# Performance work log

Hardware: AMD Instinct MI355X
Metric: run time of the kernel (lower is better)

Reference implementation:

```python
import jax, jax.numpy as jnp
import numpy as np

NPG = 100          # nodes per graph
NUM_GRAPHS = 500
N = NPG * NUM_GRAPHS
DEG = 32
E = N * DEG
IN_DIM = 100
HID = 64           # out_channels / hidden_dim
HEADS = 2
NCLS = 2


def setup_inputs() -> dict:
    key = jax.random.key(0)
    ks = jax.random.split(key, 24)
    rng = np.random.default_rng(0)
    # edges within each graph, guaranteed no self-loops
    dst = np.repeat(np.arange(N), DEG)
    off = rng.integers(1, NPG, size=E)
    src = (dst // NPG) * NPG + ((dst % NPG) + off) % NPG
    edge_index = jnp.asarray(np.stack([src, dst]).astype(np.int32))
    batch = jnp.asarray((np.arange(N) // NPG).astype(np.int32))
    HC = HEADS * HID
    p = lambda k, sh: jax.random.normal(k, sh, jnp.float32) * 0.1
    return dict(
        x=jax.random.normal(ks[0], (N, IN_DIM), jnp.float32),
        edge_attr=jax.random.uniform(ks[1], (E,), jnp.float32),
        W1=p(ks[2], (IN_DIM, HC)), as1=p(ks[3], (HEADS, HID)), ad1=p(ks[4], (HEADS, HID)), bg1=p(ks[5], (HC,)),
        l1W=p(ks[6], (HC, HID)), l1b=p(ks[7], (HID,)), g1=jnp.ones((HID,), jnp.float32), b1=jnp.zeros((HID,), jnp.float32),
        W2=p(ks[8], (HID, HC)), as2=p(ks[9], (HEADS, HID)), ad2=p(ks[10], (HEADS, HID)), bg2=p(ks[11], (HC,)),
        l2W=p(ks[12], (HC, HID)), l2b=p(ks[13], (HID,)), g2=jnp.ones((HID,), jnp.float32), b2=jnp.zeros((HID,), jnp.float32),
        f1W=p(ks[14], (HID, HID)), f1b=p(ks[15], (HID,)),
        f2W=p(ks[16], (HID, HID // 2)), f2b=p(ks[17], (HID // 2,)),
        f3W=p(ks[18], (HID // 2, NCLS)), f3b=p(ks[19], (NCLS,)),
        edge_index=edge_index, batch=batch)


def reference(x, edge_attr, W1, as1, ad1, bg1, l1W, l1b, g1, b1,
              W2, as2, ad2, bg2, l2W, l2b, g2, b2,
              f1W, f1b, f2W, f2b, f3W, f3b, edge_index, batch):
    n = x.shape[0]
    ea = jnp.abs(edge_attr)  # computed as in forward; unused by attention_weighted variant
    # GATConv adds self-loops (fill doesn't matter for alpha-only message)
    sl = jnp.arange(n, dtype=edge_index.dtype)
    src = jnp.concatenate([edge_index[0], sl])
    dst = jnp.concatenate([edge_index[1], sl])
    lrelu = lambda z: jax.nn.leaky_relu(z, 0.2)

    def gat(h, W, a_s, a_d, bias):
        xp = (h @ W).reshape(n, HEADS, HID)                 # [N,H,C]
        e = lrelu(jnp.sum(xp * a_s, -1)[src] + jnp.sum(xp * a_d, -1)[dst])  # [E',H]
        m = jax.ops.segment_max(e, dst, num_segments=n)
        ex = jnp.exp(e - m[dst])
        alpha = ex / jax.ops.segment_sum(ex, dst, num_segments=n)[dst]      # edge softmax per dst
        out = jax.ops.segment_sum(xp[src] * alpha[:, :, None], dst, num_segments=n)
        return out.reshape(n, HEADS * HID) + bias

    def bn(z, g, b):  # BatchNorm1d with batch statistics (biased var, eps=1e-5)
        return (z - z.mean(0)) * jax.lax.rsqrt(z.var(0) + 1e-5) * g + b

    z = bn(lrelu(gat(x, W1, as1, ad1, bg1) @ l1W + l1b), g1, b1)
    z = bn(lrelu(gat(z, W2, as2, ad2, bg2) @ l2W + l2b), g2, b2)
    # global mean pool
    s = jax.ops.segment_sum(z, batch, num_segments=NUM_GRAPHS)
    cnt = jax.ops.segment_sum(jnp.ones((n, 1), z.dtype), batch, num_segments=NUM_GRAPHS)
    z = s / cnt
    z = lrelu(z @ f1W + f1b)
    z = lrelu(z @ f2W + f2b)
    return z @ f3W + f3b
```

## Files before the change

kernel.cpp:

```cpp
#include <hip/hip_runtime.h>

#define NN 50000
#define NPGc 100
#define NG 500
#define DEG 32
#define HC 128
#define HID 64

__device__ __forceinline__ float lrelu(float x) { return x > 0.0f ? x : 0.2f * x; }

__global__ void k_prep(const float* __restrict__ W1, const float* __restrict__ as1,
                       const float* __restrict__ ad1, float* __restrict__ Wa1,
                       const float* __restrict__ W2, const float* __restrict__ as2,
                       const float* __restrict__ ad2, float* __restrict__ Wa2) {
  const float* W  = blockIdx.x ? W2 : W1;
  const float* as_ = blockIdx.x ? as2 : as1;
  const float* ad_ = blockIdx.x ? ad2 : ad1;
  float* Wa = blockIdx.x ? Wa2 : Wa1;
  int K = blockIdx.x ? 64 : 100;
  int t = threadIdx.x;
  for (int u = t; u < K * 4; u += blockDim.x) {
    int k = u >> 2, s = u & 3;
    const float* a = (s < 2) ? as_ : ad_;
    int h = s & 1;
    float acc = 0.f;
    for (int c = 0; c < 64; ++c) acc += W[k * 128 + h * 64 + c] * a[h * 64 + c];
    Wa[k * 4 + s] = acc;
  }
}

template <int K, bool BN>
__global__ __launch_bounds__(256) void k_layer(
    const float* __restrict__ in, const float* __restrict__ W,
    const float* __restrict__ Wa, const float* __restrict__ AB,
    const int* __restrict__ esrc, const float* __restrict__ bg,
    float* __restrict__ gout) {
  constexpr int KP = (K % 32 == 0) ? K + 4 : K;
  __shared__ __align__(16) float xph[NPGc * 64];
  __shared__ __align__(16) char ubuf[NPGc * KP * 4];
  float* xin = (float*)ubuf;
  unsigned short* srcl = (unsigned short*)ubuf;
  float* sc = (float*)(ubuf + 6400);
  float* alpha = (float*)(ubuf + 7232);

  int t = threadIdx.x;
  int g = blockIdx.x >> 1, h = blockIdx.x & 1;
  int base = g * NPGc;

  constexpr int RQ = K / 4;
  for (int u = t; u < NPGc * RQ; u += 256) {
    int r = u / RQ, q = u % RQ;
    float4 v = ((const float4*)(in + (size_t)(base + r) * K))[q];
    if (BN) {
      float4 a4 = ((const float4*)AB)[q];
      float4 b4 = ((const float4*)(AB + 64))[q];
      v.x = v.x * a4.x + b4.x; v.y = v.y * a4.y + b4.y;
      v.z = v.z * a4.z + b4.z; v.w = v.w * a4.w + b4.w;
    }
    ((float4*)(xin + r * KP))[q] = v;
  }
  __syncthreads();

  int ng = t >> 4, cg = t & 15;
  {
    float4 acc[7];
#pragma unroll
    for (int i = 0; i < 7; ++i) acc[i] = make_float4(0.f, 0.f, 0.f, 0.f);
    const float4* W4 = (const float4*)W;
    float4 w4 = W4[h * 16 + cg];
    for (int k = 0; k < K; ++k) {
      float4 wc = w4;
      if (k + 1 < K) w4 = W4[(k + 1) * 32 + h * 16 + cg];
#pragma unroll
      for (int i = 0; i < 7; ++i) {
        int r = ng + 16 * i;
        if (r < NPGc) {
          float a = xin[r * KP + k];
          acc[i].x += a * wc.x; acc[i].y += a * wc.y;
          acc[i].z += a * wc.z; acc[i].w += a * wc.w;
        }
      }
    }
#pragma unroll
    for (int i = 0; i < 7; ++i) {
      int r = ng + 16 * i;
      if (r < NPGc) ((float4*)xph)[r * 16 + cg] = acc[i];
    }
  }
  float myscore = 0.f;
  if (t < 200) {
    int node = t >> 1, s = t & 1;
    for (int k = 0; k < K; ++k) myscore += xin[node * KP + k] * Wa[k * 4 + s * 2 + h];
  }
  __syncthreads();

  if (t < 200) sc[(t & 1) * NPGc + (t >> 1)] = myscore;
  for (int u = t; u < NPGc * DEG; u += 256)
    srcl[u] = (unsigned short)(esrc[base * DEG + u] - base);
  __syncthreads();

  if (t < NPGc) {
    float sd = sc[NPGc + t];
    float es = lrelu(sc[t] + sd);
    float m = es;
    float e[DEG];
#pragma unroll
    for (int j = 0; j < DEG; ++j) {
      e[j] = lrelu(sc[srcl[t * DEG + j]] + sd);
      m = fmaxf(m, e[j]);
    }
    float exs = __expf(es - m);
    float den = exs;
#pragma unroll
    for (int j = 0; j < DEG; ++j) { e[j] = __expf(e[j] - m); den += e[j]; }
    float inv = 1.0f / den;
    float* al = alpha + t * (DEG + 2);
#pragma unroll
    for (int j = 0; j < DEG; ++j) al[j] = e[j] * inv;
    al[DEG] = exs * inv;
  }
  __syncthreads();

  float4 bgv = ((const float4*)bg)[h * 16 + cg];
  for (int d = ng; d < NPGc; d += 16) {
    const float* al = alpha + d * (DEG + 2);
    const unsigned short* sp = srcl + d * DEG;
    float aself = al[DEG];
    float4 x4 = ((float4*)xph)[d * 16 + cg];
    float4 acc;
    acc.x = aself * x4.x; acc.y = aself * x4.y;
    acc.z = aself * x4.z; acc.w = aself * x4.w;
#pragma unroll 8
    for (int j = 0; j < DEG; ++j) {
      float a = al[j];
      float4 v = ((float4*)xph)[(int)sp[j] * 16 + cg];
      acc.x += a * v.x; acc.y += a * v.y;
      acc.z += a * v.z; acc.w += a * v.w;
    }
    acc.x += bgv.x; acc.y += bgv.y; acc.z += bgv.z; acc.w += bgv.w;
    ((float4*)gout)[(size_t)(base + d) * 32 + h * 16 + cg] = acc;
  }
}

__global__ __launch_bounds__(256) void k_out_gemm(
    const float* __restrict__ gin, const float* __restrict__ lW,
    const float* __restrict__ lb, float* __restrict__ h,
    float* __restrict__ partial) {
  __shared__ __align__(16) float gl[64 * 132];
  __shared__ float psum[2 * HID];
  int t = threadIdx.x;
  int n0 = blockIdx.x * 64;

  for (int u = t; u < 64 * 32; u += 256) {
    int r = u >> 5, q = u & 31;
    int n = n0 + r;
    float4 v = make_float4(0.f, 0.f, 0.f, 0.f);
    if (n < NN) v = ((const float4*)(gin + (size_t)n * HC))[q];
    ((float4*)(gl + r * 132))[q] = v;
  }
  if (t < 2 * HID) psum[t] = 0.f;
  __syncthreads();

  int ng = t >> 4, cg = t & 15;
  int r0 = ng * 4;
  float4 acc[4];
#pragma unroll
  for (int i = 0; i < 4; ++i) acc[i] = make_float4(0.f, 0.f, 0.f, 0.f);

  const float4* lW4 = (const float4*)lW;
  float4 w4 = lW4[cg];
  for (int k = 0; k < HC; ++k) {
    float4 wc = w4;
    if (k + 1 < HC) w4 = lW4[(k + 1) * 16 + cg];
#pragma unroll
    for (int i = 0; i < 4; ++i) {
      float a = gl[(r0 + i) * 132 + k];
      acc[i].x += a * wc.x; acc[i].y += a * wc.y;
      acc[i].z += a * wc.z; acc[i].w += a * wc.w;
    }
  }
  float4 bias = ((const float4*)lb)[cg];
  float s0 = 0, s1 = 0, s2 = 0, s3 = 0, q0 = 0, q1 = 0, q2 = 0, q3 = 0;
#pragma unroll
  for (int i = 0; i < 4; ++i) {
    int n = n0 + r0 + i;
    if (n < NN) {
      float4 v;
      v.x = lrelu(acc[i].x + bias.x); v.y = lrelu(acc[i].y + bias.y);
      v.z = lrelu(acc[i].z + bias.z); v.w = lrelu(acc[i].w + bias.w);
      ((float4*)(h + (size_t)n * HID))[cg] = v;
      s0 += v.x; q0 += v.x * v.x; s1 += v.y; q1 += v.y * v.y;
      s2 += v.z; q2 += v.z * v.z; s3 += v.w; q3 += v.w * v.w;
    }
  }
  int c0 = cg * 4;
  atomicAdd(&psum[c0 + 0], s0); atomicAdd(&psum[c0 + 1], s1);
  atomicAdd(&psum[c0 + 2], s2); atomicAdd(&psum[c0 + 3], s3);
  atomicAdd(&psum[HID + c0 + 0], q0); atomicAdd(&psum[HID + c0 + 1], q1);
  atomicAdd(&psum[HID + c0 + 2], q2); atomicAdd(&psum[HID + c0 + 3], q3);
  __syncthreads();
  if (t < 2 * HID) partial[blockIdx.x * 128 + t] = psum[t];
}

__global__ __launch_bounds__(256) void k_stats(
    const float* __restrict__ partial, int nb, const float* __restrict__ gamma,
    const float* __restrict__ beta, float* __restrict__ AB) {
  __shared__ float red[2][256];
  int c = blockIdx.x, t = threadIdx.x;
  float s = 0.f, sq = 0.f;
  for (int i = t; i < nb; i += 256) {
    s += partial[i * 128 + c];
    sq += partial[i * 128 + 64 + c];
  }
  red[0][t] = s; red[1][t] = sq;
  __syncthreads();
  for (int o = 128; o > 0; o >>= 1) {
    if (t < o) { red[0][t] += red[0][t + o]; red[1][t] += red[1][t + o]; }
    __syncthreads();
  }
  if (t == 0) {
    float mean = red[0][0] / (float)NN;
    float var = red[1][0] / (float)NN - mean * mean;
    float A = gamma[c] * rsqrtf(var + 1e-5f);
    AB[c] = A;
    AB[64 + c] = beta[c] - mean * A;
  }
}

__global__ __launch_bounds__(64) void k_pool_mlp(
    const float* __restrict__ h2, const float* __restrict__ AB,
    const float* __restrict__ f1W, const float* __restrict__ f1b,
    const float* __restrict__ f2W, const float* __restrict__ f2b,
    const float* __restrict__ f3W, const float* __restrict__ f3b,
    float* __restrict__ out) {
  __shared__ float pp[4 * 64];
  __shared__ float pooled[64];
  __shared__ float z1[64];
  __shared__ float z2[32];
  int g = blockIdx.x, t = threadIdx.x;
  const float4* hb4 = (const float4*)(h2 + (size_t)g * NPGc * HID);
  int rq = t >> 4, c4 = t & 15;
  float4 s4 = make_float4(0.f, 0.f, 0.f, 0.f);
  for (int r = rq; r < NPGc; r += 4) {
    float4 v = hb4[r * 16 + c4];
    s4.x += v.x; s4.y += v.y; s4.z += v.z; s4.w += v.w;
  }
  ((float4*)pp)[rq * 16 + c4] = s4;
  __syncthreads();
  pooled[t] = (pp[t] + pp[64 + t] + pp[128 + t] + pp[192 + t]) * (1.0f / NPGc) * AB[t] + AB[64 + t];
  __syncthreads();
  float a = f1b[t];
  for (int c = 0; c < 64; ++c) a += pooled[c] * f1W[c * 64 + t];
  z1[t] = lrelu(a);
  __syncthreads();
  if (t < 32) {
    float a2 = f2b[t];
    for (int c = 0; c < 64; ++c) a2 += z1[c] * f2W[c * 32 + t];
    z2[t] = lrelu(a2);
  }
  __syncthreads();
  if (t < 2) {
    float a3 = f3b[t];
    for (int c = 0; c < 32; ++c) a3 += z2[c] * f3W[c * 2 + t];
    out[g * 2 + t] = a3;
  }
}

extern "C" void kernel_launch(void* const* d_in, const int* in_sizes, int n_in,
                              void* d_out, int out_size, void* d_ws, size_t ws_size,
                              hipStream_t stream) {
  const float* x   = (const float*)d_in[0];
  const float* W1  = (const float*)d_in[2];
  const float* as1 = (const float*)d_in[3];
  const float* ad1 = (const float*)d_in[4];
  const float* bg1 = (const float*)d_in[5];
  const float* l1W = (const float*)d_in[6];
  const float* l1b = (const float*)d_in[7];
  const float* g1  = (const float*)d_in[8];
  const float* b1  = (const float*)d_in[9];
  const float* W2  = (const float*)d_in[10];
  const float* as2 = (const float*)d_in[11];
  const float* ad2 = (const float*)d_in[12];
  const float* bg2 = (const float*)d_in[13];
  const float* l2W = (const float*)d_in[14];
  const float* l2b = (const float*)d_in[15];
  const float* g2  = (const float*)d_in[16];
  const float* b2  = (const float*)d_in[17];
  const float* f1W = (const float*)d_in[18];
  const float* f1b = (const float*)d_in[19];
  const float* f2W = (const float*)d_in[20];
  const float* f2b = (const float*)d_in[21];
  const float* f3W = (const float*)d_in[22];
  const float* f3b = (const float*)d_in[23];
  const int* esrc  = (const int*)d_in[24];
  float* out = (float*)d_out;

  float* ws = (float*)d_ws;
  size_t off = 0;
  auto alloc = [&](size_t nf) { float* p = ws + off; off += (nf + 63) & ~(size_t)63; return p; };
  float* Wa1     = alloc(100 * 4);
  float* Wa2     = alloc(64 * 4);
  float* gout    = alloc((size_t)NN * HC);
  float* hbuf    = alloc((size_t)NN * HID);
  const int NB = (NN + 63) / 64;
  float* partial = alloc((size_t)NB * 128);
  float* AB1     = alloc(128);
  float* AB2     = alloc(128);
  (void)in_sizes; (void)n_in; (void)out_size; (void)ws_size;

  k_prep<<<2, 256, 0, stream>>>(W1, as1, ad1, Wa1, W2, as2, ad2, Wa2);
  k_layer<100, false><<<NG * 2, 256, 0, stream>>>(x, W1, Wa1, nullptr, esrc, bg1, gout);
  k_out_gemm<<<NB, 256, 0, stream>>>(gout, l1W, l1b, hbuf, partial);
  k_stats<<<64, 256, 0, stream>>>(partial, NB, g1, b1, AB1);
  k_layer<64, true><<<NG * 2, 256, 0, stream>>>(hbuf, W2, Wa2, AB1, esrc, bg2, gout);
  k_out_gemm<<<NB, 256, 0, stream>>>(gout, l2W, l2b, hbuf, partial);
  k_stats<<<64, 256, 0, stream>>>(partial, NB, g2, b2, AB2);
  k_pool_mlp<<<NG, 64, 0, stream>>>(hbuf, AB2, f1W, f1b, f2W, f2b, f3W, f3b, out);
}
```

Before: 344.2 us.

## Stage GAT input in two K-chunks to shrink LDS and unroll GEMM loops by four

The per-graph GAT layer kernel now loads the input features in two column chunks into a smaller shared buffer and accumulates the projection and attention scores chunk by chunk. This cuts LDS usage per block, which could let more blocks fit on each CU. The cost is an extra barrier round. The weight-load prefetch in both the layer GEMM and the output GEMM is unrolled by four, giving more loads in flight per iteration, and the partial-row tail check is hoisted out of the inner loop.

```diff
diff --git a/kernel.cpp b/kernel.cpp
--- a/kernel.cpp
+++ b/kernel.cpp
@@ -35,10 +35,13 @@
     const float* __restrict__ Wa, const float* __restrict__ AB,
     const int* __restrict__ esrc, const float* __restrict__ bg,
     float* __restrict__ gout) {
-  constexpr int KP = (K % 32 == 0) ? K + 4 : K;
+  constexpr int CH = (K == 100) ? 52 : 32;
+  constexpr int SP = (K == 100) ? 56 : 36;
+  constexpr int XBB = NPGc * SP * 4;
+  constexpr int UBB = (XBB > 20832) ? XBB : 20832;
   __shared__ __align__(16) float xph[NPGc * 64];
-  __shared__ __align__(16) char ubuf[NPGc * KP * 4];
-  float* xin = (float*)ubuf;
+  __shared__ __align__(16) char ubuf[UBB];
+  float* xbuf = (float*)ubuf;
   unsigned short* srcl = (unsigned short*)ubuf;
   float* sc = (float*)(ubuf + 6400);
   float* alpha = (float*)(ubuf + 7232);
@@ -46,53 +49,74 @@
   int t = threadIdx.x;
   int g = blockIdx.x >> 1, h = blockIdx.x & 1;
   int base = g * NPGc;
-
-  constexpr int RQ = K / 4;
-  for (int u = t; u < NPGc * RQ; u += 256) {
-    int r = u / RQ, q = u % RQ;
-    float4 v = ((const float4*)(in + (size_t)(base + r) * K))[q];
-    if (BN) {
-      float4 a4 = ((const float4*)AB)[q];
-      float4 b4 = ((const float4*)(AB + 64))[q];
-      v.x = v.x * a4.x + b4.x; v.y = v.y * a4.y + b4.y;
-      v.z = v.z * a4.z + b4.z; v.w = v.w * a4.w + b4.w;
-    }
-    ((float4*)(xin + r * KP))[q] = v;
-  }
-  __syncthreads();
-
   int ng = t >> 4, cg = t & 15;
-  {
-    float4 acc[7];
-#pragma unroll
-    for (int i = 0; i < 7; ++i) acc[i] = make_float4(0.f, 0.f, 0.f, 0.f);
-    const float4* W4 = (const float4*)W;
-    float4 w4 = W4[h * 16 + cg];
-    for (int k = 0; k < K; ++k) {
-      float4 wc = w4;
-      if (k + 1 < K) w4 = W4[(k + 1) * 32 + h * 16 + cg];
-#pragma unroll
-      for (int i = 0; i < 7; ++i) {
-        int r = ng + 16 * i;
-        if (r < NPGc) {
-          float a = xin[r * KP + k];
-          acc[i].x += a * wc.x; acc[i].y += a * wc.y;
-          acc[i].z += a * wc.z; acc[i].w += a * wc.w;
+  int wo = h * 16 + cg;
+
+  float4 acc[7];
+#pragma unroll
+  for (int i = 0; i < 7; ++i) acc[i] = make_float4(0.f, 0.f, 0.f, 0.f);
+  float myscore = 0.f;
+  const float4* W4 = (const float4*)W;
+  const float4* in4 = (const float4*)in;
+
+#pragma unroll
+  for (int c = 0; c < 2; ++c) {
+    const int k0 = c ? CH : 0;
+    const int cols = c ? (K - CH) : CH;
+    const int QC = cols / 4;
+    for (int u = t; u < NPGc * QC; u += 256) {
+      int r = u / QC, q = u % QC;
+      float4 v = in4[(size_t)(base + r) * (K / 4) + k0 / 4 + q];
+      if (BN) {
+        float4 a4 = ((const float4*)AB)[k0 / 4 + q];
+        float4 b4 = ((const float4*)(AB + 64))[k0 / 4 + q];
+        v.x = v.x * a4.x + b4.x; v.y = v.y * a4.y + b4.y;
+        v.z = v.z * a4.z + b4.z; v.w = v.w * a4.w + b4.w;
+      }
+      ((float4*)(xbuf + r * SP))[q] = v;
+    }
+    __syncthreads();
+
+#define FMASTEP(kk_, w_) { \
+    _Pragma("unroll") \
+    for (int i = 0; i < 6; ++i) { \
+      float a_ = xbuf[(ng + 16 * i) * SP + (kk_)]; \
+      acc[i].x += a_ * w_.x; acc[i].y += a_ * w_.y; \
+      acc[i].z += a_ * w_.z; acc[i].w += a_ * w_.w; } \
+    if (ng < 4) { float a_ = xbuf[(ng + 96) * SP + (kk_)]; \
+      acc[6].x += a_ * w_.x; acc[6].y += a_ * w_.y; \
+      acc[6].z += a_ * w_.z; acc[6].w += a_ * w_.w; } }
+
+    {
+      float4 w0 = W4[(k0 + 0) * 32 + wo];
+      float4 w1 = W4[(k0 + 1) * 32 + wo];
+      float4 w2 = W4[(k0 + 2) * 32 + wo];
+      float4 w3 = W4[(k0 + 3) * 32 + wo];
+      for (int kk = 0; kk < cols; kk += 4) {
+        int kn = k0 + kk + 4;
+        bool more = (kk + 4) < cols;
+        float4 n0, n1, n2, n3;
+        if (more) {
+          n0 = W4[(kn + 0) * 32 + wo]; n1 = W4[(kn + 1) * 32 + wo];
+          n2 = W4[(kn + 2) * 32 + wo]; n3 = W4[(kn + 3) * 32 + wo];
         }
+        FMASTEP(kk + 0, w0) FMASTEP(kk + 1, w1)
+        FMASTEP(kk + 2, w2) FMASTEP(kk + 3, w3)
+        if (more) { w0 = n0; w1 = n1; w2 = n2; w3 = n3; }
       }
     }
-#pragma unroll
-    for (int i = 0; i < 7; ++i) {
-      int r = ng + 16 * i;
-      if (r < NPGc) ((float4*)xph)[r * 16 + cg] = acc[i];
-    }
-  }
-  float myscore = 0.f;
-  if (t < 200) {
-    int node = t >> 1, s = t & 1;
-    for (int k = 0; k < K; ++k) myscore += xin[node * KP + k] * Wa[k * 4 + s * 2 + h];
-  }
-  __syncthreads();
+#undef FMASTEP
+    if (t < 200) {
+      int node = t >> 1, s = t & 1;
+      for (int kk = 0; kk < cols; ++kk)
+        myscore += xbuf[node * SP + kk] * Wa[(k0 + kk) * 4 + s * 2 + h];
+    }
+    __syncthreads();
+  }
+
+#pragma unroll
+  for (int i = 0; i < 6; ++i) ((float4*)xph)[(ng + 16 * i) * 16 + cg] = acc[i];
+  if (ng < 4) ((float4*)xph)[(ng + 96) * 16 + cg] = acc[6];
 
   if (t < 200) sc[(t & 1) * NPGc + (t >> 1)] = myscore;
   for (int u = t; u < NPGc * DEG; u += 256)
@@ -127,18 +151,18 @@
     const unsigned short* sp = srcl + d * DEG;
     float aself = al[DEG];
     float4 x4 = ((float4*)xph)[d * 16 + cg];
-    float4 acc;
-    acc.x = aself * x4.x; acc.y = aself * x4.y;
-    acc.z = aself * x4.z; acc.w = aself * x4.w;
+    float4 a2;
+    a2.x = aself * x4.x; a2.y = aself * x4.y;
+    a2.z = aself * x4.z; a2.w = aself * x4.w;
 #pragma unroll 8
     for (int j = 0; j < DEG; ++j) {
       float a = al[j];
       float4 v = ((float4*)xph)[(int)sp[j] * 16 + cg];
-      acc.x += a * v.x; acc.y += a * v.y;
-      acc.z += a * v.z; acc.w += a * v.w;
-    }
-    acc.x += bgv.x; acc.y += bgv.y; acc.z += bgv.z; acc.w += bgv.w;
-    ((float4*)gout)[(size_t)(base + d) * 32 + h * 16 + cg] = acc;
+      a2.x += a * v.x; a2.y += a * v.y;
+      a2.z += a * v.z; a2.w += a * v.w;
+    }
+    a2.x += bgv.x; a2.y += bgv.y; a2.z += bgv.z; a2.w += bgv.w;
+    ((float4*)gout)[(size_t)(base + d) * 32 + h * 16 + cg] = a2;
   }
 }
 
@@ -167,18 +191,32 @@
 #pragma unroll
   for (int i = 0; i < 4; ++i) acc[i] = make_float4(0.f, 0.f, 0.f, 0.f);
 
+#define OSTEP(k_, w_) { \
+  _Pragma("unroll") \
+  for (int i = 0; i < 4; ++i) { \
+    float a_ = gl[(r0 + i) * 132 + (k_)]; \
+    acc[i].x += a_ * w_.x; acc[i].y += a_ * w_.y; \
+    acc[i].z += a_ * w_.z; acc[i].w += a_ * w_.w; } }
+
   const float4* lW4 = (const float4*)lW;
-  float4 w4 = lW4[cg];
-  for (int k = 0; k < HC; ++k) {
-    float4 wc = w4;
-    if (k + 1 < HC) w4 = lW4[(k + 1) * 16 + cg];
-#pragma unroll
-    for (int i = 0; i < 4; ++i) {
-      float a = gl[(r0 + i) * 132 + k];
-      acc[i].x += a * wc.x; acc[i].y += a * wc.y;
-      acc[i].z += a * wc.z; acc[i].w += a * wc.w;
-    }
-  }
+  {
+    float4 w0 = lW4[0 * 16 + cg];
+    float4 w1 = lW4[1 * 16 + cg];
+    float4 w2 = lW4[2 * 16 + cg];
+    float4 w3 = lW4[3 * 16 + cg];
+    for (int k = 0; k < HC; k += 4) {
+      int kn = k + 4;
+      bool more = kn < HC;
+      float4 n0, n1, n2, n3;
+      if (more) {
+        n0 = lW4[(kn + 0) * 16 + cg]; n1 = lW4[(kn + 1) * 16 + cg];
+        n2 = lW4[(kn + 2) * 16 + cg]; n3 = lW4[(kn + 3) * 16 + cg];
+      }
+      OSTEP(k + 0, w0) OSTEP(k + 1, w1) OSTEP(k + 2, w2) OSTEP(k + 3, w3)
+      if (more) { w0 = n0; w1 = n1; w2 = n2; w3 = n3; }
+    }
+  }
+#undef OSTEP
   float4 bias = ((const float4*)lb)[cg];
   float s0 = 0, s1 = 0, s2 = 0, s3 = 0, q0 = 0, q1 = 0, q2 = 0, q3 = 0;
 #pragma unroll
```

Measured after the change: 466.9 us. 1.36x slower.
